# Performance work log

Measured on AMD Instinct MI355X. Metric: run time of the kernel, lower is better.

The kernel has to match this reference:

```python
import jax, jax.numpy as jnp
import numpy as np

S, B, D, F = 2048, 8, 1024, 4096
EPS = 1e-5

def setup_inputs() -> dict:
    key = jax.random.key(0)
    ks = jax.random.split(key, 16)
    sc = lambda fan_in: 1.0 / np.sqrt(fan_in)
    inp = {
        'src': jax.random.normal(ks[0], (S, B, D), dtype=jnp.float32),
        'wq': jax.random.uniform(ks[1], (D, D), jnp.float32, -sc(D), sc(D)),
        'bq': jnp.zeros((D,), jnp.float32),
        'wk': jax.random.uniform(ks[2], (D, D), jnp.float32, -sc(D), sc(D)),
        'bk': jnp.zeros((D,), jnp.float32),
        'wv': jax.random.uniform(ks[3], (D, D), jnp.float32, -sc(D), sc(D)),
        'bv': jnp.zeros((D,), jnp.float32),
        'wo': jax.random.uniform(ks[4], (D, D), jnp.float32, -sc(D), sc(D)),
        'bo': jnp.zeros((D,), jnp.float32),
        'w1': jax.random.uniform(ks[5], (F, D), jnp.float32, -sc(D), sc(D)),
        'b1': jnp.zeros((F,), jnp.float32),
        'w2': jax.random.uniform(ks[6], (D, F), jnp.float32, -sc(F), sc(F)),
        'b2': jnp.zeros((D,), jnp.float32),
        'g1': jnp.ones((D,), jnp.float32),
        'be1': jnp.zeros((D,), jnp.float32),
        'g2': jnp.ones((D,), jnp.float32),
        'be2': jnp.zeros((D,), jnp.float32),
    }
    return inp

def _layer_norm(x, g, b):
    mu = jnp.mean(x, axis=-1, keepdims=True)
    var = jnp.mean(jnp.square(x - mu), axis=-1, keepdims=True)
    return (x - mu) / jnp.sqrt(var + EPS) * g + b

def _forward(src, wq, bq, wk, bk, wv, bv, wo, bo, w1, b1, w2, b2, g1, be1, g2, be2):
    # Linear attention (ELU+1 feature map, no normalizer — faithful to source)
    Q = jax.nn.elu(src @ wq.T + bq) + 1.0  # [S,B,D]
    K = jax.nn.elu(src @ wk.T + bk) + 1.0  # [S,B,D]
    V = src @ wv.T + bv                    # [S,B,D]
    KV = jnp.einsum('sbd,sbe->bde', K, V)  # [B,D,D]
    attn = jnp.einsum('sbd,bde->sbe', Q, KV)  # [S,B,D]
    attn = attn @ wo.T + bo
    x = _layer_norm(src + attn, g1, be1)   # dropout is identity (p=0 / eval)
    ffn = jax.nn.relu(x @ w1.T + b1) @ w2.T + b2
    return _layer_norm(x + ffn, g2, be2)

def reference(src, wq, bq, wk, bk, wv, bv, wo, bo, w1, b1, w2, b2, g1, be1, g2, be2):
    return _forward(src, wq, bq, wk, bk, wv, bv, wo, bo, w1, b1, w2, b2, g1, be1, g2, be2)
```

## Files before the change

kernel.cpp:

```cpp
#include <hip/hip_runtime.h>
#include <hip/hip_bf16.h>
#include <math.h>


typedef __attribute__((ext_vector_type(8))) short short8;
typedef __attribute__((ext_vector_type(4))) short short4_t;
typedef __attribute__((ext_vector_type(4))) float f32x4;

#define S_DIM 2048
#define B_DIM 8
#define D_DIM 1024
#define F_DIM 4096

__device__ __forceinline__ unsigned short f2bf(float f) {
  __hip_bfloat16 h = __float2bfloat16(f);
  return *reinterpret_cast<unsigned short*>(&h);
}

#define GLD16(gp, sp)                                              \
  __builtin_amdgcn_global_load_lds(                                \
      (const __attribute__((address_space(1))) void*)(gp),         \
      (__attribute__((address_space(3))) void*)(sp), 16, 0, 0)

#define BAR()                                  \
  do {                                         \
    asm volatile("" ::: "memory");             \
    __builtin_amdgcn_s_barrier();              \
    asm volatile("" ::: "memory");             \
  } while (0)
#define WAITVM4() asm volatile("s_waitcnt vmcnt(4)" ::: "memory")
#define WAITVM0() asm volatile("s_waitcnt vmcnt(0)" ::: "memory")
#define SCHED_FENCE() __builtin_amdgcn_sched_barrier(0)

template <int EPI>
__global__ __launch_bounds__(512, 2) void gemm256_kernel(
    const unsigned short* __restrict__ A, long lda, long sA,
    const unsigned short* __restrict__ B, long ldb, long sB,
    void* __restrict__ Cv, long ldc, long sC,
    const float* __restrict__ bias,
    const float* __restrict__ resid, long ldr, long sR, int K) {
  __shared__ short lds[65536];
  const int gx = gridDim.x;
  const int nwg = gx * gridDim.y;
  const int orig = blockIdx.y * gx + blockIdx.x;
  const int cpx = nwg >> 3;
  const int wgid = (orig & 7) * cpx + (orig >> 3);
  const int bx = wgid % gx, by = wgid / gx;
  const int bz = blockIdx.z;
  const unsigned short* Ablk = A + (long)bz * sA + (long)by * 256 * lda;
  const unsigned short* Bblk = B + (long)bz * sB + (long)bx * 256 * ldb;

  const int tid = threadIdx.x;
  const int w = tid >> 6, lane = tid & 63;
  const int wm = w >> 2, wn = w & 3;
  const int lr = lane & 15, kh = lane >> 4;

  const int sr = w * 8 + (lane >> 3);
  const int sc = ((lane & 7) ^ (lane >> 3)) * 8;
  const long aoff0 = (long)sr * lda + sc;
  const long aoff1 = (long)(128 + sr) * lda + sc;
  const int br0 = sr + ((sr >> 5) << 5);
  const int br1 = (64 + sr) + (((64 + sr) >> 5) << 5);
  const long boff0 = (long)br0 * ldb + sc;
  const long boff1 = (long)br1 * ldb + sc;
  const int dst0 = w * 1024;
  const int dst1 = (8 + w) * 1024;

#define STAGE_A(bufOff, h, kt)                                                \
  do {                                                                        \
    const unsigned short* _g = Ablk + (long)(h) * 64 * lda + (long)(kt) * 64; \
    GLD16(_g + aoff0, (char*)lds + (bufOff) + (h)*16384 + dst0);              \
    GLD16(_g + aoff1, (char*)lds + (bufOff) + (h)*16384 + dst1);              \
  } while (0)
#define STAGE_B(bufOff, nh, kt)                                               \
  do {                                                                        \
    const unsigned short* _g = Bblk + (long)(nh) * 32 * ldb + (long)(kt) * 64;\
    GLD16(_g + boff0, (char*)lds + (bufOff) + 32768 + (nh)*16384 + dst0);     \
    GLD16(_g + boff1, (char*)lds + (bufOff) + 32768 + (nh)*16384 + dst1);     \
  } while (0)

  const int chk0 = ((kh ^ (lr & 7)) << 4);
  const int chk1 = (((4 + kh) ^ (lr & 7)) << 4);
  const int aRdBase = (wm * 64 + lr) * 128;
  const int bRdBase = (wn * 32 + lr) * 128;

  short8 af[4][2], b0r[2][2], b1r[2][2];
  f32x4 acc[8][4];
#pragma unroll
  for (int m = 0; m < 8; ++m)
#pragma unroll
    for (int n = 0; n < 4; ++n)
#pragma unroll
      for (int j = 0; j < 4; ++j) acc[m][n][j] = 0.f;

#define LDA_H(bufOff, h)                                                     \
  do {                                                                       \
    const char* _p = (const char*)lds + (bufOff) + (h)*16384 + aRdBase;      \
    _Pragma("unroll") for (int m = 0; m < 4; ++m) {                          \
      af[m][0] = *(const short8*)(_p + m * 2048 + chk0);                     \
      af[m][1] = *(const short8*)(_p + m * 2048 + chk1);                     \
    }                                                                        \
  } while (0)
#define LDB_H(dst, bufOff, nh)                                               \
  do {                                                                       \
    const char* _p = (const char*)lds + (bufOff) + 32768 + (nh)*16384 + bRdBase; \
    _Pragma("unroll") for (int n = 0; n < 2; ++n) {                          \
      dst[n][0] = *(const short8*)(_p + n * 2048 + chk0);                    \
      dst[n][1] = *(const short8*)(_p + n * 2048 + chk1);                    \
    }                                                                        \
  } while (0)
#define MFMA_Q(mh, nh, bset)                                                 \
  do {                                                                       \
    SCHED_FENCE();                                                           \
    __builtin_amdgcn_s_setprio(1);                                           \
    _Pragma("unroll") for (int m = 0; m < 4; ++m)                            \
    _Pragma("unroll") for (int n = 0; n < 2; ++n)                            \
    _Pragma("unroll") for (int ks = 0; ks < 2; ++ks)                         \
      acc[(mh)*4 + m][(nh)*2 + n] = __builtin_amdgcn_mfma_f32_16x16x32_bf16( \
          af[m][ks], bset[n][ks], acc[(mh)*4 + m][(nh)*2 + n], 0, 0, 0);     \
    __builtin_amdgcn_s_setprio(0);                                           \
    SCHED_FENCE();                                                           \
  } while (0)

  const int T = K >> 6;
  STAGE_A(0, 0, 0); STAGE_B(0, 0, 0); STAGE_A(0, 1, 0); STAGE_B(0, 1, 0);
  STAGE_A(65536, 0, 1); STAGE_B(65536, 1, 1);
  WAITVM4();
  BAR();

  for (int i = 0; i < (T >> 1); ++i) {
    const int kt1 = 2 * i + 1;
    const int ktn0 = (2 * i + 2 < T) ? (2 * i + 2) : (T - 1);
    const int ktn1 = (2 * i + 3 < T) ? (2 * i + 3) : (T - 1);
    LDA_H(0, 0); LDB_H(b0r, 0, 0); STAGE_A(65536, 1, kt1);
    BAR(); MFMA_Q(0, 0, b0r); BAR();
    LDB_H(b1r, 0, 1); STAGE_B(65536, 0, kt1);
    BAR(); MFMA_Q(0, 1, b1r); BAR();
    LDA_H(0, 1); STAGE_A(0, 0, ktn0);
    BAR(); MFMA_Q(1, 1, b1r); BAR();
    STAGE_B(0, 1, ktn0);
    WAITVM4(); BAR(); MFMA_Q(1, 0, b0r); BAR();
    LDA_H(65536, 0); LDB_H(b0r, 65536, 0); STAGE_A(0, 1, ktn0);
    BAR(); MFMA_Q(0, 0, b0r); BAR();
    LDB_H(b1r, 65536, 1); STAGE_B(0, 0, ktn0);
    BAR(); MFMA_Q(0, 1, b1r); BAR();
    LDA_H(65536, 1); STAGE_A(65536, 0, ktn1);
    BAR(); MFMA_Q(1, 1, b1r); BAR();
    STAGE_B(65536, 1, ktn1);
    WAITVM4(); BAR(); MFMA_Q(1, 0, b0r); BAR();
  }
  WAITVM0();

  const long gm0 = (long)by * 256 + wm * 128;
  const long gn0 = (long)bx * 256 + wn * 64;
  if constexpr (EPI == 4) {
    float* C = (float*)Cv + (long)bz * sC;
    const float* R = resid + (long)bz * sR;
#pragma unroll
    for (int mg = 0; mg < 8; ++mg)
#pragma unroll
      for (int ng = 0; ng < 4; ++ng) {
        const long col = gn0 + ng * 16 + lr;
        const float bcol = bias[col];
#pragma unroll
        for (int j = 0; j < 4; ++j) {
          const long row = gm0 + mg * 16 + kh * 4 + j;
          C[row * ldc + col] = acc[mg][ng][j] + bcol + R[row * ldr + col];
        }
      }
  } else {
    unsigned short* C = (unsigned short*)Cv + (long)bz * sC;
#pragma unroll
    for (int mg = 0; mg < 8; ++mg)
#pragma unroll
      for (int ng = 0; ng < 4; ++ng) {
        const long col = gn0 + ng * 16 + lr;
        const float bcol = bias[col];
#pragma unroll
        for (int j = 0; j < 4; ++j) {
          const long row = gm0 + mg * 16 + kh * 4 + j;
          float v = acc[mg][ng][j] + bcol;
          if constexpr (EPI == 1) v = (v > 0.f) ? (v + 1.f) : expf(v);
          if constexpr (EPI == 3) v = fmaxf(v, 0.f);
          C[row * ldc + col] = f2bf(v);
        }
      }
  }
#undef STAGE_A
#undef STAGE_B
#undef LDA_H
#undef LDB_H
#undef MFMA_Q
}

template <int EPI>
__global__ __launch_bounds__(256, 2) void gemm_bt_kernel(
    const unsigned short* __restrict__ A, long lda, long sA,
    const unsigned short* __restrict__ B, long ldb, long sB,
    void* __restrict__ Cv, long ldc, long sC,
    const float* __restrict__ bias,
    const float* __restrict__ resid, long ldr, long sR, int K) {
  __shared__ short As[128 * 32];
  __shared__ short Bs[128 * 32];
  const int gx = gridDim.x;
  const int nwg = gx * gridDim.y;
  const int orig = blockIdx.y * gx + blockIdx.x;
  const int cpx = nwg >> 3;
  const int wgid = (orig & 7) * cpx + (orig >> 3);
  const int bx = wgid % gx;
  const int by = wgid / gx;

  const int bz = blockIdx.z;
  const unsigned short* Ab = A + (long)bz * sA + (long)by * 128 * lda;
  const unsigned short* Bb = B + (long)bz * sB + (long)bx * 128 * ldb;
  const int tid = threadIdx.x;
  const int w = tid >> 6, lane = tid & 63;
  const int srow = lane >> 2;
  const int scol = (lane & 3) * 8;
  const int wr = (w >> 1) * 64, wc = (w & 1) * 64;
  const int lr = lane & 15, kh = lane >> 4;

  f32x4 acc[4][4];
#pragma unroll
  for (int m = 0; m < 4; ++m)
#pragma unroll
    for (int n = 0; n < 4; ++n)
#pragma unroll
      for (int j = 0; j < 4; ++j) acc[m][n][j] = 0.f;

  const unsigned short* ga0 = Ab + (long)(w * 16 + srow) * lda + scol;
  const unsigned short* ga1 = Ab + (long)(64 + w * 16 + srow) * lda + scol;
  const unsigned short* gb0 = Bb + (long)(w * 16 + srow) * ldb + scol;
  const unsigned short* gb1 = Bb + (long)(64 + w * 16 + srow) * ldb + scol;
  short* la0 = &As[(w * 16) * 32];
  short* la1 = &As[(64 + w * 16) * 32];
  short* lb0 = &Bs[(w * 16) * 32];
  short* lb1 = &Bs[(64 + w * 16) * 32];

  for (int k0 = 0; k0 < K; k0 += 32) {
    GLD16(ga0 + k0, la0);
    GLD16(ga1 + k0, la1);
    GLD16(gb0 + k0, lb0);
    GLD16(gb1 + k0, lb1);
    __syncthreads();
    short8 af[4], bf[4];
#pragma unroll
    for (int m = 0; m < 4; ++m)
      af[m] = *(const short8*)&As[(wr + m * 16 + lr) * 32 + kh * 8];
#pragma unroll
    for (int n = 0; n < 4; ++n)
      bf[n] = *(const short8*)&Bs[(wc + n * 16 + lr) * 32 + kh * 8];
#pragma unroll
    for (int m = 0; m < 4; ++m)
#pragma unroll
      for (int n = 0; n < 4; ++n)
        acc[m][n] =
            __builtin_amdgcn_mfma_f32_16x16x32_bf16(af[m], bf[n], acc[m][n], 0, 0, 0);
    __syncthreads();
  }

  const long gm0 = (long)by * 128 + wr;
  const long gn0 = (long)bx * 128 + wc;
  unsigned short* C = (unsigned short*)Cv + (long)bz * sC;
#pragma unroll
  for (int m = 0; m < 4; ++m)
#pragma unroll
    for (int n = 0; n < 4; ++n) {
      const long col = gn0 + n * 16 + lr;
#pragma unroll
      for (int j = 0; j < 4; ++j) {
        const long row = gm0 + m * 16 + kh * 4 + j;
        C[row * ldc + col] = f2bf(acc[m][n][j]);
      }
    }
}

__global__ __launch_bounds__(256) void transpose_kernel(
    const unsigned short* __restrict__ in, unsigned short* __restrict__ out) {
  __shared__ unsigned short t[64][68];
  const int b = blockIdx.z;
  const long s0 = (long)blockIdx.x * 64, d0 = (long)blockIdx.y * 64;
  const int tid = threadIdx.x;
  {
    const int r = tid >> 3, c = (tid & 7) * 8;
#pragma unroll
    for (int it = 0; it < 2; ++it) {
      const int s = r + it * 32;
      const unsigned short* g = &in[(s0 + s) * (B_DIM * D_DIM) + (long)b * D_DIM + d0 + c];
      short4_t v0 = *(const short4_t*)g;
      short4_t v1 = *(const short4_t*)(g + 4);
      *(short4_t*)&t[s][c] = v0;
      *(short4_t*)&t[s][c + 4] = v1;
    }
  }
  __syncthreads();
  {
    const int d = tid >> 3, c = (tid & 7) * 8;
#pragma unroll
    for (int it = 0; it < 2; ++it) {
      const int dd = d + it * 32;
      short8 v;
#pragma unroll
      for (int j = 0; j < 8; ++j) v[j] = (short)t[c + j][dd];
      *(short8*)&out[(long)b * ((long)D_DIM * S_DIM) + (d0 + dd) * S_DIM + s0 + c] = v;
    }
  }
}

template <int WRITE_BF16>
__global__ __launch_bounds__(256) void layernorm_kernel(
    const float* in, float* outf, unsigned short* __restrict__ outb,
    const float* __restrict__ gamma, const float* __restrict__ beta) {
  const long row = blockIdx.x;
  const float* x = in + row * D_DIM;
  const int tid = threadIdx.x;
  const int lane = tid & 63, w = tid >> 6;
  f32x4 v = *(const f32x4*)&x[tid * 4];
  float s = v[0] + v[1] + v[2] + v[3];
  float q = v[0] * v[0] + v[1] * v[1] + v[2] * v[2] + v[3] * v[3];
#pragma unroll
  for (int off = 32; off > 0; off >>= 1) {
    s += __shfl_down(s, off, 64);
    q += __shfl_down(q, off, 64);
  }
  __shared__ float red[8];
  if (lane == 0) { red[w] = s; red[w + 4] = q; }
  __syncthreads();
  s = red[0] + red[1] + red[2] + red[3];
  q = red[4] + red[5] + red[6] + red[7];
  const float mu = s * (1.f / D_DIM);
  const float var = q * (1.f / D_DIM) - mu * mu;
  const float rs = rsqrtf(var + 1e-5f);
  f32x4 g = *(const f32x4*)&gamma[tid * 4];
  f32x4 bb = *(const f32x4*)&beta[tid * 4];
  f32x4 o;
#pragma unroll
  for (int j = 0; j < 4; ++j) o[j] = (v[j] - mu) * rs * g[j] + bb[j];
  *(f32x4*)&outf[row * D_DIM + tid * 4] = o;
  if constexpr (WRITE_BF16) {
    short4_t ob;
#pragma unroll
    for (int j = 0; j < 4; ++j) ob[j] = (short)f2bf(o[j]);
    *(short4_t*)&outb[row * D_DIM + tid * 4] = ob;
  }
}

__global__ __launch_bounds__(256) void cast_kernel(
    const float* __restrict__ in, unsigned short* __restrict__ out, long n) {
  long i = ((long)blockIdx.x * 256 + threadIdx.x) * 8;
  if (i >= n) return;
  f32x4 a = *(const f32x4*)&in[i];
  f32x4 b = *(const f32x4*)&in[i + 4];
  short8 v;
#pragma unroll
  for (int j = 0; j < 4; ++j) v[j] = (short)f2bf(a[j]);
#pragma unroll
  for (int j = 0; j < 4; ++j) v[4 + j] = (short)f2bf(b[j]);
  *(short8*)&out[i] = v;
}

extern "C" void kernel_launch(void* const* d_in, const int* in_sizes, int n_in,
                              void* d_out, int out_size, void* d_ws, size_t ws_size,
                              hipStream_t stream) {
  const float* src = (const float*)d_in[0];
  const float* wq  = (const float*)d_in[1];
  const float* bq  = (const float*)d_in[2];
  const float* wk  = (const float*)d_in[3];
  const float* bk  = (const float*)d_in[4];
  const float* wv  = (const float*)d_in[5];
  const float* bv  = (const float*)d_in[6];
  const float* wo  = (const float*)d_in[7];
  const float* bo  = (const float*)d_in[8];
  const float* w1  = (const float*)d_in[9];
  const float* b1  = (const float*)d_in[10];
  const float* w2  = (const float*)d_in[11];
  const float* b2  = (const float*)d_in[12];
  const float* g1  = (const float*)d_in[13];
  const float* be1 = (const float*)d_in[14];
  const float* g2  = (const float*)d_in[15];
  const float* be2 = (const float*)d_in[16];

  const long MB = 1024L * 1024L;
  if (ws_size < 248 * MB) return;
  char* ws = (char*)d_ws;
  unsigned short* w1b  = (unsigned short*)(ws + 0 * MB);
  unsigned short* w2b  = (unsigned short*)(ws + 8 * MB);
  float*          X    = (float*)(ws + 16 * MB);
  unsigned short* Xb   = (unsigned short*)(ws + 80 * MB);
  unsigned short* H    = (unsigned short*)(ws + 112 * MB);
  unsigned short* wqb  = (unsigned short*)(ws + 112 * MB);
  unsigned short* wkb  = (unsigned short*)(ws + 114 * MB);
  unsigned short* wvb  = (unsigned short*)(ws + 116 * MB);
  unsigned short* wob  = (unsigned short*)(ws + 118 * MB);
  unsigned short* srcb = (unsigned short*)(ws + 120 * MB);
  unsigned short* Kt   = (unsigned short*)(ws + 120 * MB);
  unsigned short* Vt   = (unsigned short*)(ws + 16 * MB);
  unsigned short* KVm  = (unsigned short*)(ws + 48 * MB);
  unsigned short* Mt   = (unsigned short*)(ws + 64 * MB);
  unsigned short* Qb   = (unsigned short*)(ws + 152 * MB);
  unsigned short* Kb   = (unsigned short*)(ws + 184 * MB);
  unsigned short* Vb   = (unsigned short*)(ws + 216 * MB);
  float*          AO   = (float*)(ws + 184 * MB);

  const dim3 blk(256);
  const dim3 blk512(512);
  cast_kernel<<<dim3(512), blk, 0, stream>>>(wq, wqb, 1048576);
  cast_kernel<<<dim3(512), blk, 0, stream>>>(wk, wkb, 1048576);
  cast_kernel<<<dim3(512), blk, 0, stream>>>(wv, wvb, 1048576);
  cast_kernel<<<dim3(512), blk, 0, stream>>>(wo, wob, 1048576);
  cast_kernel<<<dim3(2048), blk, 0, stream>>>(w1, w1b, 4194304);
  cast_kernel<<<dim3(2048), blk, 0, stream>>>(w2, w2b, 4194304);
  cast_kernel<<<dim3(8192), blk, 0, stream>>>(src, srcb, 16777216);

  gemm256_kernel<1><<<dim3(4, 64, 1), blk512, 0, stream>>>(
      srcb, 1024, 0, wqb, 1024, 0, Qb, 1024, 0, bq, nullptr, 0, 0, 1024);
  gemm256_kernel<1><<<dim3(4, 64, 1), blk512, 0, stream>>>(
      srcb, 1024, 0, wkb, 1024, 0, Kb, 1024, 0, bk, nullptr, 0, 0, 1024);
  gemm256_kernel<2><<<dim3(4, 64, 1), blk512, 0, stream>>>(
      srcb, 1024, 0, wvb, 1024, 0, Vb, 1024, 0, bv, nullptr, 0, 0, 1024);

  transpose_kernel<<<dim3(32, 16, 8), blk, 0, stream>>>(Kb, Kt);
  transpose_kernel<<<dim3(32, 16, 8), blk, 0, stream>>>(Vb, Vt);

  gemm_bt_kernel<0><<<dim3(8, 8, 8), blk, 0, stream>>>(
      Kt, 2048, 2097152, Vt, 2048, 2097152, KVm, 1024, 1048576,
      nullptr, nullptr, 0, 0, 2048);
  gemm_bt_kernel<0><<<dim3(8, 8, 8), blk, 0, stream>>>(
      wob, 1024, 0, KVm, 1024, 1048576, Mt, 1024, 1048576,
      nullptr, nullptr, 0, 0, 1024);
  gemm256_kernel<4><<<dim3(4, 8, 8), blk512, 0, stream>>>(
      Qb, 8192, 1024, Mt, 1024, 1048576, AO, 8192, 1024,
      bo, src, 8192, 1024, 1024);

  layernorm_kernel<1><<<dim3(16384), blk, 0, stream>>>(AO, X, Xb, g1, be1);

  gemm256_kernel<3><<<dim3(16, 64, 1), blk512, 0, stream>>>(
      Xb, 1024, 0, w1b, 1024, 0, H, 4096, 0, b1, nullptr, 0, 0, 1024);
  gemm256_kernel<4><<<dim3(4, 64, 1), blk512, 0, stream>>>(
      H, 4096, 0, w2b, 4096, 0, (float*)d_out, 1024, 0,
      b2, X, 1024, 0, 4096);

  layernorm_kernel<0><<<dim3(16384), blk, 0, stream>>>(
      (float*)d_out, (float*)d_out, nullptr, g2, be2);
}
```

Baseline: 646.7 us.

## Fuse Q/K/V projections into one GEMM and rework the LDS staging schedule

Concatenates wq, wk and wv (and their biases) into one 3072-wide weight, so a single GEMM produces an interleaved QKV buffer, with ELU+1 applied only to the Q and K column ranges. The transpose and attention-output GEMM now read Q, K and V from that buffer with strides. The main GEMM's prefetch order and vmcnt waits are also changed to keep more global-to-LDS loads in flight and to wait more often. This cuts kernel launches and re-reads of src, and the larger grid fills the device better, at the cost of more complex workspace aliasing and strided reads.

```diff
diff --git a/kernel.cpp b/kernel.cpp
--- a/kernel.cpp
+++ b/kernel.cpp
@@ -28,7 +28,7 @@
     __builtin_amdgcn_s_barrier();              \
     asm volatile("" ::: "memory");             \
   } while (0)
-#define WAITVM4() asm volatile("s_waitcnt vmcnt(4)" ::: "memory")
+#define WAITVM10() asm volatile("s_waitcnt vmcnt(10)" ::: "memory")
 #define WAITVM0() asm volatile("s_waitcnt vmcnt(0)" ::: "memory")
 #define SCHED_FENCE() __builtin_amdgcn_sched_barrier(0)
 
@@ -123,31 +123,30 @@
   } while (0)
 
   const int T = K >> 6;
-  STAGE_A(0, 0, 0); STAGE_B(0, 0, 0); STAGE_A(0, 1, 0); STAGE_B(0, 1, 0);
-  STAGE_A(65536, 0, 1); STAGE_B(65536, 1, 1);
-  WAITVM4();
-  BAR();
+  STAGE_A(0, 0, 0); STAGE_B(0, 0, 0); STAGE_B(0, 1, 0); STAGE_A(0, 1, 0);
+  STAGE_A(65536, 0, 1); STAGE_B(65536, 0, 1); STAGE_B(65536, 1, 1);
+  WAITVM10(); BAR();
 
   for (int i = 0; i < (T >> 1); ++i) {
-    const int kt1 = 2 * i + 1;
-    const int ktn0 = (2 * i + 2 < T) ? (2 * i + 2) : (T - 1);
-    const int ktn1 = (2 * i + 3 < T) ? (2 * i + 3) : (T - 1);
-    LDA_H(0, 0); LDB_H(b0r, 0, 0); STAGE_A(65536, 1, kt1);
-    BAR(); MFMA_Q(0, 0, b0r); BAR();
-    LDB_H(b1r, 0, 1); STAGE_B(65536, 0, kt1);
-    BAR(); MFMA_Q(0, 1, b1r); BAR();
-    LDA_H(0, 1); STAGE_A(0, 0, ktn0);
+    const int kto  = 2 * i + 1;
+    const int kte2 = (2 * i + 2 < T) ? (2 * i + 2) : (T - 1);
+    const int kto2 = (2 * i + 3 < T) ? (2 * i + 3) : (T - 1);
+    LDA_H(0, 0); LDB_H(b0r, 0, 0); STAGE_A(65536, 1, kto);
+    WAITVM10(); BAR(); MFMA_Q(0, 0, b0r); BAR();
+    LDB_H(b1r, 0, 1); STAGE_A(0, 0, kte2);
+    WAITVM10(); BAR(); MFMA_Q(0, 1, b1r); BAR();
+    LDA_H(0, 1); STAGE_B(0, 0, kte2);
     BAR(); MFMA_Q(1, 1, b1r); BAR();
-    STAGE_B(0, 1, ktn0);
-    WAITVM4(); BAR(); MFMA_Q(1, 0, b0r); BAR();
-    LDA_H(65536, 0); LDB_H(b0r, 65536, 0); STAGE_A(0, 1, ktn0);
-    BAR(); MFMA_Q(0, 0, b0r); BAR();
-    LDB_H(b1r, 65536, 1); STAGE_B(0, 0, ktn0);
-    BAR(); MFMA_Q(0, 1, b1r); BAR();
-    LDA_H(65536, 1); STAGE_A(65536, 0, ktn1);
+    STAGE_B(0, 1, kte2);
+    WAITVM10(); BAR(); MFMA_Q(1, 0, b0r); BAR();
+    LDA_H(65536, 0); LDB_H(b0r, 65536, 0); STAGE_A(0, 1, kte2);
+    WAITVM10(); BAR(); MFMA_Q(0, 0, b0r); BAR();
+    LDB_H(b1r, 65536, 1); STAGE_A(65536, 0, kto2);
+    WAITVM10(); BAR(); MFMA_Q(0, 1, b1r); BAR();
+    LDA_H(65536, 1); STAGE_B(65536, 0, kto2);
     BAR(); MFMA_Q(1, 1, b1r); BAR();
-    STAGE_B(65536, 1, ktn1);
-    WAITVM4(); BAR(); MFMA_Q(1, 0, b0r); BAR();
+    STAGE_B(65536, 1, kto2);
+    WAITVM10(); BAR(); MFMA_Q(1, 0, b0r); BAR();
   }
   WAITVM0();
 
@@ -170,6 +169,7 @@
       }
   } else {
     unsigned short* C = (unsigned short*)Cv + (long)bz * sC;
+    const bool do_elu = (EPI == 5) && (gn0 < 2048);
 #pragma unroll
     for (int mg = 0; mg < 8; ++mg)
 #pragma unroll
@@ -180,8 +180,10 @@
         for (int j = 0; j < 4; ++j) {
           const long row = gm0 + mg * 16 + kh * 4 + j;
           float v = acc[mg][ng][j] + bcol;
-          if constexpr (EPI == 1) v = (v > 0.f) ? (v + 1.f) : expf(v);
           if constexpr (EPI == 3) v = fmaxf(v, 0.f);
+          if constexpr (EPI == 5) {
+            if (do_elu) v = (v > 0.f) ? (v + 1.f) : expf(v);
+          }
           C[row * ldc + col] = f2bf(v);
         }
       }
@@ -276,7 +278,8 @@
 }
 
 __global__ __launch_bounds__(256) void transpose_kernel(
-    const unsigned short* __restrict__ in, unsigned short* __restrict__ out) {
+    const unsigned short* __restrict__ in, unsigned short* __restrict__ out,
+    long ld) {
   __shared__ unsigned short t[64][68];
   const int b = blockIdx.z;
   const long s0 = (long)blockIdx.x * 64, d0 = (long)blockIdx.y * 64;
@@ -286,7 +289,7 @@
 #pragma unroll
     for (int it = 0; it < 2; ++it) {
       const int s = r + it * 32;
-      const unsigned short* g = &in[(s0 + s) * (B_DIM * D_DIM) + (long)b * D_DIM + d0 + c];
+      const unsigned short* g = &in[((s0 + s) * B_DIM + b) * ld + d0 + c];
       short4_t v0 = *(const short4_t*)g;
       short4_t v1 = *(const short4_t*)(g + 4);
       *(short4_t*)&t[s][c] = v0;
@@ -383,44 +386,40 @@
   const long MB = 1024L * 1024L;
   if (ws_size < 248 * MB) return;
   char* ws = (char*)d_ws;
-  unsigned short* w1b  = (unsigned short*)(ws + 0 * MB);
-  unsigned short* w2b  = (unsigned short*)(ws + 8 * MB);
-  float*          X    = (float*)(ws + 16 * MB);
-  unsigned short* Xb   = (unsigned short*)(ws + 80 * MB);
-  unsigned short* H    = (unsigned short*)(ws + 112 * MB);
-  unsigned short* wqb  = (unsigned short*)(ws + 112 * MB);
-  unsigned short* wkb  = (unsigned short*)(ws + 114 * MB);
-  unsigned short* wvb  = (unsigned short*)(ws + 116 * MB);
-  unsigned short* wob  = (unsigned short*)(ws + 118 * MB);
-  unsigned short* srcb = (unsigned short*)(ws + 120 * MB);
-  unsigned short* Kt   = (unsigned short*)(ws + 120 * MB);
-  unsigned short* Vt   = (unsigned short*)(ws + 16 * MB);
-  unsigned short* KVm  = (unsigned short*)(ws + 48 * MB);
-  unsigned short* Mt   = (unsigned short*)(ws + 64 * MB);
-  unsigned short* Qb   = (unsigned short*)(ws + 152 * MB);
-  unsigned short* Kb   = (unsigned short*)(ws + 184 * MB);
-  unsigned short* Vb   = (unsigned short*)(ws + 216 * MB);
-  float*          AO   = (float*)(ws + 184 * MB);
+  unsigned short* w1b   = (unsigned short*)(ws + 0 * MB);
+  unsigned short* w2b   = (unsigned short*)(ws + 8 * MB);
+  unsigned short* srcb  = (unsigned short*)(ws + 16 * MB);
+  unsigned short* Kt    = (unsigned short*)(ws + 16 * MB);
+  unsigned short* Vt    = (unsigned short*)(ws + 48 * MB);
+  float*          AO    = (float*)(ws + 16 * MB);
+  float*          X     = (float*)(ws + 16 * MB);
+  unsigned short* KVm   = (unsigned short*)(ws + 80 * MB);
+  unsigned short* Mt    = (unsigned short*)(ws + 96 * MB);
+  unsigned short* Xb    = (unsigned short*)(ws + 80 * MB);
+  unsigned short* wqkvb = (unsigned short*)(ws + 112 * MB);
+  float*          bqkv  = (float*)(ws + 118 * MB);
+  unsigned short* wob   = (unsigned short*)(ws + 119 * MB);
+  unsigned short* QKVb  = (unsigned short*)(ws + 144 * MB);
+  unsigned short* H     = (unsigned short*)(ws + 112 * MB);
 
   const dim3 blk(256);
   const dim3 blk512(512);
-  cast_kernel<<<dim3(512), blk, 0, stream>>>(wq, wqb, 1048576);
-  cast_kernel<<<dim3(512), blk, 0, stream>>>(wk, wkb, 1048576);
-  cast_kernel<<<dim3(512), blk, 0, stream>>>(wv, wvb, 1048576);
+  cast_kernel<<<dim3(512), blk, 0, stream>>>(wq, wqkvb, 1048576);
+  cast_kernel<<<dim3(512), blk, 0, stream>>>(wk, wqkvb + 1048576, 1048576);
+  cast_kernel<<<dim3(512), blk, 0, stream>>>(wv, wqkvb + 2097152, 1048576);
   cast_kernel<<<dim3(512), blk, 0, stream>>>(wo, wob, 1048576);
   cast_kernel<<<dim3(2048), blk, 0, stream>>>(w1, w1b, 4194304);
   cast_kernel<<<dim3(2048), blk, 0, stream>>>(w2, w2b, 4194304);
   cast_kernel<<<dim3(8192), blk, 0, stream>>>(src, srcb, 16777216);
-
-  gemm256_kernel<1><<<dim3(4, 64, 1), blk512, 0, stream>>>(
-      srcb, 1024, 0, wqb, 1024, 0, Qb, 1024, 0, bq, nullptr, 0, 0, 1024);
-  gemm256_kernel<1><<<dim3(4, 64, 1), blk512, 0, stream>>>(
-      srcb, 1024, 0, wkb, 1024, 0, Kb, 1024, 0, bk, nullptr, 0, 0, 1024);
-  gemm256_kernel<2><<<dim3(4, 64, 1), blk512, 0, stream>>>(
-      srcb, 1024, 0, wvb, 1024, 0, Vb, 1024, 0, bv, nullptr, 0, 0, 1024);
-
-  transpose_kernel<<<dim3(32, 16, 8), blk, 0, stream>>>(Kb, Kt);
-  transpose_kernel<<<dim3(32, 16, 8), blk, 0, stream>>>(Vb, Vt);
+  hipMemcpyAsync(bqkv, bq, 4096, hipMemcpyDeviceToDevice, stream);
+  hipMemcpyAsync(bqkv + 1024, bk, 4096, hipMemcpyDeviceToDevice, stream);
+  hipMemcpyAsync(bqkv + 2048, bv, 4096, hipMemcpyDeviceToDevice, stream);
+
+  gemm256_kernel<5><<<dim3(12, 64, 1), blk512, 0, stream>>>(
+      srcb, 1024, 0, wqkvb, 1024, 0, QKVb, 3072, 0, bqkv, nullptr, 0, 0, 1024);
+
+  transpose_kernel<<<dim3(32, 16, 8), blk, 0, stream>>>(QKVb + 1024, Kt, 3072);
+  transpose_kernel<<<dim3(32, 16, 8), blk, 0, stream>>>(QKVb + 2048, Vt, 3072);
 
   gemm_bt_kernel<0><<<dim3(8, 8, 8), blk, 0, stream>>>(
       Kt, 2048, 2097152, Vt, 2048, 2097152, KVm, 1024, 1048576,
@@ -429,7 +428,7 @@
       wob, 1024, 0, KVm, 1024, 1048576, Mt, 1024, 1048576,
       nullptr, nullptr, 0, 0, 1024);
   gemm256_kernel<4><<<dim3(4, 8, 8), blk512, 0, stream>>>(
-      Qb, 8192, 1024, Mt, 1024, 1048576, AO, 8192, 1024,
+      QKVb, 24576, 3072, Mt, 1024, 1048576, AO, 8192, 1024,
       bo, src, 8192, 1024, 1024);
 
   layernorm_kernel<1><<<dim3(16384), blk, 0, stream>>>(AO, X, Xb, g1, be1);
```

New measurement: 652.5 us. Within noise of the previous version (+0.9%).
